# Kernel optimization log

Measured on AMD Instinct MI355X. Metric: run time of the kernel, lower is better.

The kernel has to match this reference:

```python
import jax, jax.numpy as jnp
import numpy as np

N = 8192      # active sparse voxels
C = 768       # model_channels
H = 12        # heads
DH = 64       # head dim
NB = 12       # blocks
WS = 8        # window size
RES = 64      # voxel grid resolution
NG = 32       # gaussians per voxel
OUT_CH = 448  # 96+96+96+128+32


def _radical_inverse(base, n):
    inv, f = 0.0, 1.0 / base
    while n > 0:
        inv += f * (n % base)
        n //= base
        f /= base
    return inv


def _hammersley(num):
    return np.array([[i / num, _radical_inverse(2, i), _radical_inverse(3, i)]
                     for i in range(num)], dtype=np.float32)


def _windows(coords, shift):
    # swin partition: window id of each voxel after shifting coords
    wc = (coords.astype(np.int64) + shift) // WS
    G = (RES + shift) // WS + 1
    wid = (wc[:, 0] * G + wc[:, 1]) * G + wc[:, 2]
    uniq, vwin, counts = np.unique(wid, return_inverse=True, return_counts=True)
    nw, cap, n = len(uniq), int(counts.max()), len(wid)
    order = np.argsort(wid, kind='stable')
    starts = np.concatenate([[0], np.cumsum(counts)[:-1]])
    slot_sorted = np.arange(n) - starts[vwin[order]]
    vslot = np.empty(n, dtype=np.int64)
    vslot[order] = slot_sorted
    idx = np.full((nw, cap), n, dtype=np.int32)  # n = padding row
    idx[vwin, vslot] = np.arange(n)
    mask = idx < n
    return (jnp.asarray(idx), jnp.asarray(mask),
            jnp.asarray(vwin.astype(np.int32)), jnp.asarray(vslot.astype(np.int32)))


def setup_inputs() -> dict:
    rng = np.random.RandomState(0)
    coords = rng.randint(0, RES, size=(N, 3)).astype(np.int32)
    feats = rng.randn(N, 8).astype(np.float32)
    idx0, mask0, vwin0, vslot0 = _windows(coords, 0)          # even blocks
    idx1, mask1, vwin1, vslot1 = _windows(coords, WS // 2)    # odd blocks (shifted)
    s = 0.02
    def w(*shape):
        return jnp.asarray((rng.randn(*shape) * s).astype(np.float32))
    perturb = _hammersley(NG) * 2.0 - 1.0
    perturb = np.arctanh(perturb / 1.5).astype(np.float32)  # voxel_size=1.5
    return dict(
        feats=jnp.asarray(feats), coords=jnp.asarray(coords),
        in_w=w(8, C), in_b=jnp.zeros((C,), jnp.float32),
        qkv_w=w(NB, C, 3 * C), qkv_b=jnp.zeros((NB, 3 * C), jnp.float32),
        proj_w=w(NB, C, C), proj_b=jnp.zeros((NB, C), jnp.float32),
        mlp_w1=w(NB, C, 4 * C), mlp_b1=jnp.zeros((NB, 4 * C), jnp.float32),
        mlp_w2=w(NB, 4 * C, C), mlp_b2=jnp.zeros((NB, C), jnp.float32),
        out_w=w(C, OUT_CH), out_b=jnp.zeros((OUT_CH,), jnp.float32),
        perturb=jnp.asarray(perturb),
        idx0=idx0, mask0=mask0, vwin0=vwin0, vslot0=vslot0,
        idx1=idx1, mask1=mask1, vwin1=vwin1, vslot1=vslot1,
    )


def _ln(x, eps):
    mu = jnp.mean(x, -1, keepdims=True)
    xc = x - mu
    var = jnp.mean(xc * xc, -1, keepdims=True)
    return xc * jax.lax.rsqrt(var + eps)


def _pos_embed(coords):
    freq_dim = C // 3 // 2  # 128
    freqs = 1.0 / (10000.0 ** (jnp.arange(freq_dim, dtype=jnp.float32) / freq_dim))
    phase = coords.astype(jnp.float32)[..., None] * freqs          # [N,3,128]
    emb = jnp.concatenate([jnp.sin(phase), jnp.cos(phase)], -1)    # [N,3,256]
    return emb.reshape(coords.shape[0], C)


def _win_attn(q, k, v, idx, mask):
    zpad = jnp.zeros((1,) + q.shape[1:], q.dtype)
    qw = jnp.concatenate([q, zpad], 0)[idx]   # [nw,cap,H,DH]
    kw = jnp.concatenate([k, zpad], 0)[idx]
    vw = jnp.concatenate([v, zpad], 0)[idx]
    scores = jnp.einsum('wihd,wjhd->whij', qw, kw) / np.float32(np.sqrt(DH))
    scores = jnp.where(mask[:, None, None, :], scores, jnp.float32(-1e9))
    attn = jax.nn.softmax(scores, axis=-1)
    return jnp.einsum('whij,wjhd->wihd', attn, vw)   # [nw,cap,H,DH]


def _forward(feats, coords, in_w, in_b, qkv_w, qkv_b, proj_w, proj_b,
             mlp_w1, mlp_b1, mlp_w2, mlp_b2, out_w, out_b, perturb,
             idx0, mask0, vwin0, vslot0, idx1, mask1, vwin1, vslot1):
    cfgs = [(idx0, mask0, vwin0, vslot0), (idx1, mask1, vwin1, vslot1)]
    n = feats.shape[0]
    h = feats @ in_w + in_b + _pos_embed(coords)
    for i in range(NB):
        idx, mask, vwin, vslot = cfgs[i % 2]
        qkv = (_ln(h, 1e-6) @ qkv_w[i] + qkv_b[i]).reshape(n, 3, H, DH)
        ow = _win_attn(qkv[:, 0], qkv[:, 1], qkv[:, 2], idx, mask)
        o = ow[vwin, vslot].reshape(n, C)
        h = h + (o @ proj_w[i] + proj_b[i])
        hid = jax.nn.gelu(_ln(h, 1e-6) @ mlp_w1[i] + mlp_b1[i], approximate=False)
        h = h + (hid @ mlp_w2[i] + mlp_b2[i])
    out = _ln(h, 1e-5) @ out_w + out_b   # F.layer_norm default eps
    # to_representation
    xyz = (coords.astype(jnp.float32) + 0.5) / RES                   # [N,3]
    off = out[:, :96].reshape(n, NG, 3)                               # lr=1.0
    off = jnp.tanh(off + perturb) / RES * 0.5 * 1.5                   # voxel_size=1.5
    g_xyz = (xyz[:, None, :] + off).reshape(n * NG, 3)
    g_dc = out[:, 96:192].reshape(n * NG, 3)
    g_scal = out[:, 192:288].reshape(n * NG, 3)
    g_rot = out[:, 288:416].reshape(n * NG, 4) * 0.1                  # lr=0.1
    g_opa = out[:, 416:448].reshape(n * NG, 1)
    return jnp.concatenate([g_xyz, g_dc, g_scal, g_rot, g_opa], -1)   # [N*32,14]


def reference(feats, coords, in_w, in_b, qkv_w, qkv_b, proj_w, proj_b,
              mlp_w1, mlp_b1, mlp_w2, mlp_b2, out_w, out_b, perturb,
              idx0, mask0, vwin0, vslot0, idx1, mask1, vwin1, vslot1):
    return _forward(feats, coords, in_w, in_b, qkv_w, qkv_b, proj_w, proj_b,
                    mlp_w1, mlp_b1, mlp_w2, mlp_b2, out_w, out_b, perturb,
                    idx0, mask0, vwin0, vslot0, idx1, mask1, vwin1, vslot1)
```

## Files before the change

kernel.cpp:

```cpp
#include <hip/hip_runtime.h>
#include <math.h>

#define NVOX 8192
#define CCH 768
#define NH 12
#define DH 64
#define NBLK 12
#define NG 32
#define OUT_CH 448
#define OUT_PAD 512
#define CAP 48
#define APITCH 72

typedef __attribute__((ext_vector_type(8))) short v8s;
typedef __attribute__((ext_vector_type(4))) float v4f;

__device__ __forceinline__ unsigned short f2bf(float f) {
  unsigned u = __builtin_bit_cast(unsigned, f);
  u += 0x7fffu + ((u >> 16) & 1u);
  return (unsigned short)(u >> 16);
}
__device__ __forceinline__ float bf2f(unsigned short b) {
  return __builtin_bit_cast(float, (unsigned)b << 16);
}

__device__ __forceinline__ void async16(const void* g, void* l) {
  __builtin_amdgcn_global_load_lds(
      (const __attribute__((address_space(1))) unsigned int*)g,
      (__attribute__((address_space(3))) unsigned int*)l, 16, 0, 0);
}

__global__ __launch_bounds__(256) void cap_kernel(const int* __restrict__ a,
                                                  const int* __restrict__ b,
                                                  int n, int* __restrict__ caps) {
  __shared__ int s0[256], s1[256];
  int m0 = 0, m1 = 0;
  for (int i = threadIdx.x; i < n; i += 256) {
    m0 = max(m0, a[i]);
    m1 = max(m1, b[i]);
  }
  s0[threadIdx.x] = m0;
  s1[threadIdx.x] = m1;
  __syncthreads();
  for (int st = 128; st > 0; st >>= 1) {
    if (threadIdx.x < st) {
      s0[threadIdx.x] = max(s0[threadIdx.x], s0[threadIdx.x + st]);
      s1[threadIdx.x] = max(s1[threadIdx.x], s1[threadIdx.x + st]);
    }
    __syncthreads();
  }
  if (threadIdx.x == 0) {
    caps[0] = s0[0] + 1;
    caps[1] = s1[0] + 1;
  }
}

__global__ __launch_bounds__(256) void embed_kernel(const float* __restrict__ feats,
                                                    const int* __restrict__ coords,
                                                    const float* __restrict__ in_w,
                                                    const float* __restrict__ in_b,
                                                    float* __restrict__ h) {
  int id = blockIdx.x * 256 + threadIdx.x;
  if (id >= NVOX * CCH) return;
  int n = id / CCH, c = id - n * CCH;
  float acc = in_b[c];
#pragma unroll
  for (int k = 0; k < 8; ++k) acc += feats[n * 8 + k] * in_w[k * CCH + c];
  int axis = c / 256;
  int r = c - axis * 256;
  int f = r & 127;
  float freq = __expf(-(float)f * (9.210340371976184f / 128.0f));
  float phase = (float)coords[n * 3 + axis] * freq;
  acc += (r < 128) ? __sinf(phase) : __cosf(phase);
  h[id] = acc;
}

__global__ __launch_bounds__(256) void ln_kernel(const float* __restrict__ x,
                                                 unsigned short* __restrict__ y,
                                                 float eps) {
  int row = blockIdx.x;
  const float* xr = x + (size_t)row * CCH;
  float v[3];
  float s = 0.f, s2 = 0.f;
#pragma unroll
  for (int j = 0; j < 3; ++j) {
    v[j] = xr[threadIdx.x + j * 256];
    s += v[j];
    s2 += v[j] * v[j];
  }
#pragma unroll
  for (int off = 32; off >= 1; off >>= 1) {
    s += __shfl_xor(s, off, 64);
    s2 += __shfl_xor(s2, off, 64);
  }
  __shared__ float ss[4], ss2[4];
  int wave = threadIdx.x >> 6, lane = threadIdx.x & 63;
  if (lane == 0) { ss[wave] = s; ss2[wave] = s2; }
  __syncthreads();
  s = ss[0] + ss[1] + ss[2] + ss[3];
  s2 = ss2[0] + ss2[1] + ss2[2] + ss2[3];
  float mu = s * (1.0f / CCH);
  float var = s2 * (1.0f / CCH) - mu * mu;
  float rr = rsqrtf(var + eps);
  unsigned short* yr = y + (size_t)row * CCH;
#pragma unroll
  for (int j = 0; j < 3; ++j) yr[threadIdx.x + j * 256] = f2bf((v[j] - mu) * rr);
}

__device__ __forceinline__ void wconv_tile(const float* __restrict__ W,
                                           unsigned short* __restrict__ Wt,
                                           int K, int Nsrc, int nt, int kt,
                                           float (*t)[65]) {
  int n0 = nt * 64, k0 = kt * 64;
  for (int e = threadIdx.x; e < 4096; e += 256) {
    int r = e >> 6, c = e & 63;
    int n = n0 + c;
    t[r][c] = (n < Nsrc) ? W[(size_t)(k0 + r) * Nsrc + n] : 0.f;
  }
  __syncthreads();
  for (int e = threadIdx.x; e < 4096; e += 256) {
    int rn = e >> 6, ck = e & 63;
    Wt[(size_t)(n0 + rn) * K + k0 + ck] = f2bf(t[ck][rn]);
  }
}

__global__ __launch_bounds__(256) void wconvert(const float* __restrict__ W,
                                                unsigned short* __restrict__ Wt,
                                                int K, int Nsrc) {
  __shared__ float t[64][65];
  wconv_tile(W, Wt, K, Nsrc, blockIdx.x, blockIdx.y, t);
}

__global__ __launch_bounds__(256) void wconvert4(const float* __restrict__ W0,
                                                 const float* __restrict__ W1,
                                                 const float* __restrict__ W2,
                                                 const float* __restrict__ W3,
                                                 unsigned short* __restrict__ D0,
                                                 unsigned short* __restrict__ D1,
                                                 unsigned short* __restrict__ D2,
                                                 unsigned short* __restrict__ D3) {
  __shared__ float t[64][65];
  int b = blockIdx.x;
  if (b < 432) {
    wconv_tile(W0, D0, 768, 2304, b / 12, b % 12, t);
  } else if (b < 576) {
    b -= 432;
    wconv_tile(W1, D1, 768, 768, b / 12, b % 12, t);
  } else if (b < 1152) {
    b -= 576;
    wconv_tile(W2, D2, 768, 3072, b / 12, b % 12, t);
  } else {
    b -= 1152;
    wconv_tile(W3, D3, 3072, 768, b / 48, b % 48, t);
  }
}

__device__ __forceinline__ float gelu_exact(float x) {
  return 0.5f * x * (1.0f + erff(x * 0.70710678118654752f));
}

template <int ACT, int RES, int OUTBF>
__global__ __launch_bounds__(256) void gemm_mfma(const unsigned short* __restrict__ A,
                                                 const unsigned short* __restrict__ Bt,
                                                 const float* __restrict__ bias, int Nbias,
                                                 float* __restrict__ outf,
                                                 unsigned short* __restrict__ outb,
                                                 int Nn, int K) {
  __shared__ __align__(16) unsigned short As[128 * 32];
  __shared__ __align__(16) unsigned short Bs[128 * 32];
  const int tid = threadIdx.x;
  const int lane = tid & 63, w = tid >> 6;
  const int row0 = blockIdx.y * 128, col0 = blockIdx.x * 128;
  const int wm = (w >> 1) * 64, wn = (w & 1) * 64;
  const int fm = lane & 15, fq = lane >> 4;

  const int c0 = w * 64 + lane;
  const int c1 = c0 + 256;
  const unsigned short* gA0 = A + (size_t)(row0 + (c0 >> 2)) * K + (c0 & 3) * 8;
  const unsigned short* gA1 = A + (size_t)(row0 + (c1 >> 2)) * K + (c1 & 3) * 8;
  const unsigned short* gB0 = Bt + (size_t)(col0 + (c0 >> 2)) * K + (c0 & 3) * 8;
  const unsigned short* gB1 = Bt + (size_t)(col0 + (c1 >> 2)) * K + (c1 & 3) * 8;
  unsigned short* lA0 = As + (size_t)(w * 64) * 8;
  unsigned short* lA1 = As + (size_t)(w * 64 + 256) * 8;
  unsigned short* lB0 = Bs + (size_t)(w * 64) * 8;
  unsigned short* lB1 = Bs + (size_t)(w * 64 + 256) * 8;

  v4f acc[4][4];
#pragma unroll
  for (int i = 0; i < 4; ++i)
#pragma unroll
    for (int j = 0; j < 4; ++j) acc[i][j] = (v4f){0.f, 0.f, 0.f, 0.f};

  for (int k0 = 0; k0 < K; k0 += 32) {
    async16(gA0 + k0, lA0);
    async16(gA1 + k0, lA1);
    async16(gB0 + k0, lB0);
    async16(gB1 + k0, lB1);
    __syncthreads();
    v8s af[4], bf[4];
#pragma unroll
    for (int i = 0; i < 4; ++i)
      af[i] = *(const v8s*)(As + (size_t)(wm + i * 16 + fm) * 32 + fq * 8);
#pragma unroll
    for (int j = 0; j < 4; ++j)
      bf[j] = *(const v8s*)(Bs + (size_t)(wn + j * 16 + fm) * 32 + fq * 8);
#pragma unroll
    for (int i = 0; i < 4; ++i)
#pragma unroll
      for (int j = 0; j < 4; ++j)
        acc[i][j] = __builtin_amdgcn_mfma_f32_16x16x32_bf16(af[i], bf[j], acc[i][j], 0, 0, 0);
    __syncthreads();
  }

#pragma unroll
  for (int i = 0; i < 4; ++i) {
    int row = row0 + wm + i * 16 + fq * 4;
#pragma unroll
    for (int j = 0; j < 4; ++j) {
      int col = col0 + wn + j * 16 + fm;
      float b = (col < Nbias) ? bias[col] : 0.f;
#pragma unroll
      for (int r = 0; r < 4; ++r) {
        float v = acc[i][j][r] + b;
        if (ACT == 1) v = gelu_exact(v);
        size_t o = (size_t)(row + r) * Nn + col;
        if (RES) {
          outf[o] += v;
        } else if (OUTBF) {
          outb[o] = f2bf(v);
        } else {
          outf[o] = v;
        }
      }
    }
  }
}

__global__ __launch_bounds__(64) void attn_kernel(const unsigned short* __restrict__ qkv,
                                                  const int* __restrict__ idx,
                                                  const int* __restrict__ capPtr,
                                                  int total,
                                                  unsigned short* __restrict__ attn_out) {
  __shared__ __align__(16) unsigned short QP[CAP * APITCH];
  __shared__ __align__(16) unsigned short Ks[CAP * APITCH];
  __shared__ __align__(16) unsigned short Vt[64 * APITCH];
  __shared__ int vox_lds[64];
  const int cap = *capPtr;
  if (cap > CAP) return;
  const int nw = total / cap;
  const int tasks = nw * NH;
  const int lane = threadIdx.x;
  const int fm = lane & 15, fq = lane >> 4;
  const v8s z8 = {0, 0, 0, 0, 0, 0, 0, 0};

  for (int task = blockIdx.x; task < tasks; task += gridDim.x) {
    const int w = task / NH, hh = task - w * NH;
    int vox_i = NVOX;
    if (lane < cap) vox_i = idx[w * cap + lane];
    vox_lds[lane] = vox_i;
    __syncthreads();

#pragma unroll
    for (int it = 0; it < 6; ++it) {
      int id = it * 64 + lane;
      int j = id >> 3, c = id & 7;
      int vj = vox_lds[j];
      v8s q8 = z8, k8 = z8;
      if (vj < NVOX) {
        const unsigned short* base = qkv + (size_t)vj * (3 * CCH) + hh * DH + c * 8;
        q8 = *(const v8s*)(base);
        k8 = *(const v8s*)(base + CCH);
      }
      *(v8s*)(QP + j * APITCH + c * 8) = q8;
      *(v8s*)(Ks + j * APITCH + c * 8) = k8;
    }
#pragma unroll 4
    for (int j = 0; j < CAP; ++j) {
      int vj = vox_lds[j];
      unsigned short vv = 0;
      if (vj < NVOX) vv = qkv[(size_t)vj * (3 * CCH) + 2 * CCH + hh * DH + lane];
      Vt[lane * APITCH + j] = vv;
    }
#pragma unroll
    for (int j = CAP; j < 64; ++j) Vt[lane * APITCH + j] = 0;
    __syncthreads();

    v4f s_acc[3][3];
#pragma unroll
    for (int mi = 0; mi < 3; ++mi)
#pragma unroll
      for (int jt = 0; jt < 3; ++jt) s_acc[mi][jt] = (v4f){0.f, 0.f, 0.f, 0.f};
#pragma unroll
    for (int ks = 0; ks < 2; ++ks) {
      v8s qf[3], kf[3];
#pragma unroll
      for (int mi = 0; mi < 3; ++mi)
        qf[mi] = *(const v8s*)(QP + (mi * 16 + fm) * APITCH + ks * 32 + fq * 8);
#pragma unroll
      for (int jt = 0; jt < 3; ++jt)
        kf[jt] = *(const v8s*)(Ks + (jt * 16 + fm) * APITCH + ks * 32 + fq * 8);
#pragma unroll
      for (int mi = 0; mi < 3; ++mi)
#pragma unroll
        for (int jt = 0; jt < 3; ++jt)
          s_acc[mi][jt] = __builtin_amdgcn_mfma_f32_16x16x32_bf16(qf[mi], kf[jt], s_acc[mi][jt], 0, 0, 0);
    }
    __syncthreads();

    bool va0 = (fm < cap) && (vox_lds[fm] < NVOX);
    bool va1 = (16 + fm < cap) && (vox_lds[16 + fm] < NVOX);
    bool va2 = (32 + fm < cap) && (vox_lds[32 + fm] < NVOX);
#pragma unroll
    for (int mi = 0; mi < 3; ++mi) {
#pragma unroll
      for (int r = 0; r < 4; ++r) {
        float e0 = va0 ? __expf(s_acc[mi][0][r] * 0.125f) : 0.f;
        float e1 = va1 ? __expf(s_acc[mi][1][r] * 0.125f) : 0.f;
        float e2 = va2 ? __expf(s_acc[mi][2][r] * 0.125f) : 0.f;
        float den = e0 + e1 + e2;
        den += __shfl_xor(den, 1, 64);
        den += __shfl_xor(den, 2, 64);
        den += __shfl_xor(den, 4, 64);
        den += __shfl_xor(den, 8, 64);
        float rden = (den > 0.f) ? 1.0f / den : 0.f;
        int row = mi * 16 + fq * 4 + r;
        QP[row * APITCH + fm] = f2bf(e0 * rden);
        QP[row * APITCH + 16 + fm] = f2bf(e1 * rden);
        QP[row * APITCH + 32 + fm] = f2bf(e2 * rden);
      }
    }
    if (lane < CAP) {
      *(v8s*)(QP + lane * APITCH + 48) = z8;
      *(v8s*)(QP + lane * APITCH + 56) = z8;
    }
    __syncthreads();

    v4f o_acc[3][4];
#pragma unroll
    for (int mi = 0; mi < 3; ++mi)
#pragma unroll
      for (int nt = 0; nt < 4; ++nt) o_acc[mi][nt] = (v4f){0.f, 0.f, 0.f, 0.f};
#pragma unroll
    for (int ks = 0; ks < 2; ++ks) {
      v8s pf[3], vf[4];
#pragma unroll
      for (int mi = 0; mi < 3; ++mi)
        pf[mi] = *(const v8s*)(QP + (mi * 16 + fm) * APITCH + ks * 32 + fq * 8);
#pragma unroll
      for (int nt = 0; nt < 4; ++nt)
        vf[nt] = *(const v8s*)(Vt + (nt * 16 + fm) * APITCH + ks * 32 + fq * 8);
#pragma unroll
      for (int mi = 0; mi < 3; ++mi)
#pragma unroll
        for (int nt = 0; nt < 4; ++nt)
          o_acc[mi][nt] = __builtin_amdgcn_mfma_f32_16x16x32_bf16(pf[mi], vf[nt], o_acc[mi][nt], 0, 0, 0);
    }

#pragma unroll
    for (int mi = 0; mi < 3; ++mi) {
#pragma unroll
      for (int r = 0; r < 4; ++r) {
        int i = mi * 16 + fq * 4 + r;
        int vox = vox_lds[i];
        if (i < cap && vox < NVOX) {
          unsigned short* ob = attn_out + (size_t)vox * CCH + hh * DH + fm;
#pragma unroll
          for (int nt = 0; nt < 4; ++nt) ob[nt * 16] = f2bf(o_acc[mi][nt][r]);
        }
      }
    }
    __syncthreads();
  }
}

__global__ __launch_bounds__(256) void decode_kernel(const float* __restrict__ outpad,
                                                     const int* __restrict__ coords,
                                                     const float* __restrict__ perturb,
                                                     float* __restrict__ out) {
  __shared__ float row[OUT_CH];
  const int n = blockIdx.x;
  const float* src = outpad + (size_t)n * OUT_PAD;
  for (int e = threadIdx.x; e < OUT_CH; e += 256) row[e] = src[e];
  __syncthreads();
  float* o = out + (size_t)n * OUT_CH;
  for (int e = threadIdx.x; e < OUT_CH; e += 256) {
    int g = e / 14, j = e - g * 14;
    float v;
    if (j < 3) {
      float xyz = ((float)coords[n * 3 + j] + 0.5f) * (1.0f / 64.0f);
      v = xyz + tanhf(row[g * 3 + j] + perturb[g * 3 + j]) * (0.75f / 64.0f);
    } else if (j < 6) {
      v = row[96 + g * 3 + (j - 3)];
    } else if (j < 9) {
      v = row[192 + g * 3 + (j - 6)];
    } else if (j < 13) {
      v = row[288 + g * 4 + (j - 9)] * 0.1f;
    } else {
      v = row[416 + g];
    }
    o[e] = v;
  }
}

extern "C" void kernel_launch(void* const* d_in, const int* in_sizes, int n_in,
                              void* d_out, int out_size, void* d_ws, size_t ws_size,
                              hipStream_t stream) {
  const float* feats = (const float*)d_in[0];
  const int* coords = (const int*)d_in[1];
  const float* in_w = (const float*)d_in[2];
  const float* in_b = (const float*)d_in[3];
  const float* qkv_w = (const float*)d_in[4];
  const float* qkv_b = (const float*)d_in[5];
  const float* proj_w = (const float*)d_in[6];
  const float* proj_b = (const float*)d_in[7];
  const float* mlp_w1 = (const float*)d_in[8];
  const float* mlp_b1 = (const float*)d_in[9];
  const float* mlp_w2 = (const float*)d_in[10];
  const float* mlp_b2 = (const float*)d_in[11];
  const float* out_w = (const float*)d_in[12];
  const float* out_b = (const float*)d_in[13];
  const float* perturb = (const float*)d_in[14];
  const int* idx0 = (const int*)d_in[15];
  const int* vslot0 = (const int*)d_in[18];
  const int* idx1 = (const int*)d_in[19];
  const int* vslot1 = (const int*)d_in[22];
  const int total0 = in_sizes[15];
  const int total1 = in_sizes[19];

  char* p = (char*)d_ws;
  int* caps = (int*)p;
  float* h = (float*)(p + 256);
  unsigned short* abuf = (unsigned short*)(p + 256 + 25165824);
  unsigned short* big = (unsigned short*)(p + 256 + 37748736);
  unsigned short* wst = (unsigned short*)(p + 256 + 88080384);
  float* outpad = (float*)(p + 256 + 102236160);
  const size_t OQ = 0;
  const size_t OP = (size_t)768 * 2304;
  const size_t OM1 = OP + (size_t)768 * 768;
  const size_t OM2 = OM1 + (size_t)768 * 3072;

  cap_kernel<<<1, 256, 0, stream>>>(vslot0, vslot1, NVOX, caps);
  embed_kernel<<<(NVOX * CCH + 255) / 256, 256, 0, stream>>>(feats, coords, in_w, in_b, h);

  for (int i = 0; i < NBLK; ++i) {
    const int* idx = (i & 1) ? idx1 : idx0;
    const int* capP = (i & 1) ? caps + 1 : caps;
    const int total = (i & 1) ? total1 : total0;

    wconvert4<<<1728, 256, 0, stream>>>(
        qkv_w + (size_t)i * 768 * 2304, proj_w + (size_t)i * 768 * 768,
        mlp_w1 + (size_t)i * 768 * 3072, mlp_w2 + (size_t)i * 3072 * 768,
        wst + OQ, wst + OP, wst + OM1, wst + OM2);

    ln_kernel<<<NVOX, 256, 0, stream>>>(h, abuf, 1e-6f);
    gemm_mfma<0, 0, 1><<<dim3(18, 64), 256, 0, stream>>>(
        abuf, wst + OQ, qkv_b + (size_t)i * 2304, 2304, nullptr, big, 2304, 768);
    attn_kernel<<<4096, 64, 0, stream>>>(big, idx, capP, total, abuf);
    gemm_mfma<0, 1, 0><<<dim3(6, 64), 256, 0, stream>>>(
        abuf, wst + OP, proj_b + (size_t)i * 768, 768, h, nullptr, 768, 768);
    ln_kernel<<<NVOX, 256, 0, stream>>>(h, abuf, 1e-6f);
    gemm_mfma<1, 0, 1><<<dim3(24, 64), 256, 0, stream>>>(
        abuf, wst + OM1, mlp_b1 + (size_t)i * 3072, 3072, nullptr, big, 3072, 768);
    gemm_mfma<0, 1, 0><<<dim3(6, 64), 256, 0, stream>>>(
        big, wst + OM2, mlp_b2 + (size_t)i * 768, 768, h, nullptr, 768, 3072);
  }

  ln_kernel<<<NVOX, 256, 0, stream>>>(h, abuf, 1e-5f);
  wconvert<<<dim3(8, 12), 256, 0, stream>>>(out_w, wst + OQ, 768, OUT_CH);
  gemm_mfma<0, 0, 0><<<dim3(4, 64), 256, 0, stream>>>(
      abuf, wst + OQ, out_b, OUT_CH, outpad, nullptr, OUT_PAD, 768);
  decode_kernel<<<NVOX, 256, 0, stream>>>(outpad, coords, perturb, (float*)d_out);
}
```

Measured before the change: 4.533 ms.

## Add split-K with atomic accumulation and double K-step per GEMM iteration

The GEMM kernel now loads a 64-wide K slab per barrier pair instead of 32, halving the number of synchronisations. It also gains a split-K mode where blockIdx.z handles a slice of K and results are atomically added into the fp32 residual. The two residual GEMMs (proj and MLP down) use 2 and 4 splits to fill more CUs, since their 6x64 grids are small. Atomics add memory traffic and make the floating-point sum order nondeterministic.

```diff
diff --git a/kernel.cpp b/kernel.cpp
--- a/kernel.cpp
+++ b/kernel.cpp
@@ -159,31 +159,38 @@
   return 0.5f * x * (1.0f + erff(x * 0.70710678118654752f));
 }
 
-template <int ACT, int RES, int OUTBF>
+template <int ACT, int RES, int OUTBF, int SPLIT>
 __global__ __launch_bounds__(256) void gemm_mfma(const unsigned short* __restrict__ A,
                                                  const unsigned short* __restrict__ Bt,
                                                  const float* __restrict__ bias, int Nbias,
                                                  float* __restrict__ outf,
                                                  unsigned short* __restrict__ outb,
                                                  int Nn, int K) {
-  __shared__ __align__(16) unsigned short As[128 * 32];
-  __shared__ __align__(16) unsigned short Bs[128 * 32];
+  __shared__ __align__(16) unsigned short As[2 * 128 * 32];
+  __shared__ __align__(16) unsigned short Bs[2 * 128 * 32];
   const int tid = threadIdx.x;
   const int lane = tid & 63, w = tid >> 6;
   const int row0 = blockIdx.y * 128, col0 = blockIdx.x * 128;
   const int wm = (w >> 1) * 64, wn = (w & 1) * 64;
   const int fm = lane & 15, fq = lane >> 4;
-
-  const int c0 = w * 64 + lane;
-  const int c1 = c0 + 256;
-  const unsigned short* gA0 = A + (size_t)(row0 + (c0 >> 2)) * K + (c0 & 3) * 8;
-  const unsigned short* gA1 = A + (size_t)(row0 + (c1 >> 2)) * K + (c1 & 3) * 8;
-  const unsigned short* gB0 = Bt + (size_t)(col0 + (c0 >> 2)) * K + (c0 & 3) * 8;
-  const unsigned short* gB1 = Bt + (size_t)(col0 + (c1 >> 2)) * K + (c1 & 3) * 8;
-  unsigned short* lA0 = As + (size_t)(w * 64) * 8;
-  unsigned short* lA1 = As + (size_t)(w * 64 + 256) * 8;
-  unsigned short* lB0 = Bs + (size_t)(w * 64) * 8;
-  unsigned short* lB1 = Bs + (size_t)(w * 64 + 256) * 8;
+  const int Kc = SPLIT ? (K / gridDim.z) : K;
+  const int kbase = SPLIT ? (blockIdx.z * Kc) : 0;
+
+  const unsigned short* gA[4];
+  const unsigned short* gB[4];
+  unsigned short* lA[4];
+  unsigned short* lB[4];
+#pragma unroll
+  for (int t = 0; t < 4; ++t) {
+    int c = t * 256 + w * 64 + lane;
+    int ks = c >> 9, cc = c & 511;
+    int r = cc >> 2, kc = cc & 3;
+    size_t koff = (size_t)kbase + ks * 32 + kc * 8;
+    gA[t] = A + (size_t)(row0 + r) * K + koff;
+    gB[t] = Bt + (size_t)(col0 + r) * K + koff;
+    lA[t] = As + (size_t)(t * 256 + w * 64) * 8;
+    lB[t] = Bs + (size_t)(t * 256 + w * 64) * 8;
+  }
 
   v4f acc[4][4];
 #pragma unroll
@@ -191,24 +198,28 @@
 #pragma unroll
     for (int j = 0; j < 4; ++j) acc[i][j] = (v4f){0.f, 0.f, 0.f, 0.f};
 
-  for (int k0 = 0; k0 < K; k0 += 32) {
-    async16(gA0 + k0, lA0);
-    async16(gA1 + k0, lA1);
-    async16(gB0 + k0, lB0);
-    async16(gB1 + k0, lB1);
-    __syncthreads();
-    v8s af[4], bf[4];
-#pragma unroll
-    for (int i = 0; i < 4; ++i)
-      af[i] = *(const v8s*)(As + (size_t)(wm + i * 16 + fm) * 32 + fq * 8);
-#pragma unroll
-    for (int j = 0; j < 4; ++j)
-      bf[j] = *(const v8s*)(Bs + (size_t)(wn + j * 16 + fm) * 32 + fq * 8);
-#pragma unroll
-    for (int i = 0; i < 4; ++i)
+  for (int k0 = 0; k0 < Kc; k0 += 64) {
+#pragma unroll
+    for (int t = 0; t < 4; ++t) {
+      async16(gA[t] + k0, lA[t]);
+      async16(gB[t] + k0, lB[t]);
+    }
+    __syncthreads();
+#pragma unroll
+    for (int ks = 0; ks < 2; ++ks) {
+      v8s af[4], bf[4];
+#pragma unroll
+      for (int i = 0; i < 4; ++i)
+        af[i] = *(const v8s*)(As + ks * 4096 + (size_t)(wm + i * 16 + fm) * 32 + fq * 8);
 #pragma unroll
       for (int j = 0; j < 4; ++j)
-        acc[i][j] = __builtin_amdgcn_mfma_f32_16x16x32_bf16(af[i], bf[j], acc[i][j], 0, 0, 0);
+        bf[j] = *(const v8s*)(Bs + ks * 4096 + (size_t)(wn + j * 16 + fm) * 32 + fq * 8);
+#pragma unroll
+      for (int i = 0; i < 4; ++i)
+#pragma unroll
+        for (int j = 0; j < 4; ++j)
+          acc[i][j] = __builtin_amdgcn_mfma_f32_16x16x32_bf16(af[i], bf[j], acc[i][j], 0, 0, 0);
+    }
     __syncthreads();
   }
 
@@ -218,13 +229,16 @@
 #pragma unroll
     for (int j = 0; j < 4; ++j) {
       int col = col0 + wn + j * 16 + fm;
-      float b = (col < Nbias) ? bias[col] : 0.f;
+      float b = 0.f;
+      if (!SPLIT || blockIdx.z == 0) b = (col < Nbias) ? bias[col] : 0.f;
 #pragma unroll
       for (int r = 0; r < 4; ++r) {
         float v = acc[i][j][r] + b;
         if (ACT == 1) v = gelu_exact(v);
         size_t o = (size_t)(row + r) * Nn + col;
-        if (RES) {
+        if (SPLIT) {
+          atomicAdd(outf + o, v);
+        } else if (RES) {
           outf[o] += v;
         } else if (OUTBF) {
           outb[o] = f2bf(v);
@@ -453,21 +467,21 @@
         wst + OQ, wst + OP, wst + OM1, wst + OM2);
 
     ln_kernel<<<NVOX, 256, 0, stream>>>(h, abuf, 1e-6f);
-    gemm_mfma<0, 0, 1><<<dim3(18, 64), 256, 0, stream>>>(
+    gemm_mfma<0, 0, 1, 0><<<dim3(18, 64), 256, 0, stream>>>(
         abuf, wst + OQ, qkv_b + (size_t)i * 2304, 2304, nullptr, big, 2304, 768);
     attn_kernel<<<4096, 64, 0, stream>>>(big, idx, capP, total, abuf);
-    gemm_mfma<0, 1, 0><<<dim3(6, 64), 256, 0, stream>>>(
+    gemm_mfma<0, 1, 0, 1><<<dim3(6, 64, 2), 256, 0, stream>>>(
         abuf, wst + OP, proj_b + (size_t)i * 768, 768, h, nullptr, 768, 768);
     ln_kernel<<<NVOX, 256, 0, stream>>>(h, abuf, 1e-6f);
-    gemm_mfma<1, 0, 1><<<dim3(24, 64), 256, 0, stream>>>(
+    gemm_mfma<1, 0, 1, 0><<<dim3(24, 64), 256, 0, stream>>>(
         abuf, wst + OM1, mlp_b1 + (size_t)i * 3072, 3072, nullptr, big, 3072, 768);
-    gemm_mfma<0, 1, 0><<<dim3(6, 64), 256, 0, stream>>>(
+    gemm_mfma<0, 1, 0, 1><<<dim3(6, 64, 4), 256, 0, stream>>>(
         big, wst + OM2, mlp_b2 + (size_t)i * 768, 768, h, nullptr, 768, 3072);
   }
 
   ln_kernel<<<NVOX, 256, 0, stream>>>(h, abuf, 1e-5f);
   wconvert<<<dim3(8, 12), 256, 0, stream>>>(out_w, wst + OQ, 768, OUT_CH);
-  gemm_mfma<0, 0, 0><<<dim3(4, 64), 256, 0, stream>>>(
+  gemm_mfma<0, 0, 0, 0><<<dim3(4, 64), 256, 0, stream>>>(
       abuf, wst + OQ, out_b, OUT_CH, outpad, nullptr, OUT_PAD, 768);
   decode_kernel<<<NVOX, 256, 0, stream>>>(outpad, coords, perturb, (float*)d_out);
 }
```

Result: slower. 4.708 ms (+3.9%).
